# Kernel optimization log

Measured on AMD Instinct MI355X. Metric: run time of the kernel, lower is better.

## Reference

```python
import jax, jax.numpy as jnp
import numpy as np

B = 262144      # batch of states (PPO rollout)
J = 16          # num_pools -> state_dim=32, action_dim=256
M = 12          # num_epochs_per_day (experts)
H = 34          # hidden_dim (fixed in source)
A = J * J


def setup_inputs() -> dict:
    key = jax.random.key(0)
    ks = jax.random.split(key, 6)
    states = jax.random.normal(ks[0], (B, 2 * J), dtype=jnp.float32)
    epoch_idx = jax.random.randint(ks[1], (B,), 0, M, dtype=jnp.int32)
    # fc1: kaiming normal (relu), zero bias
    W1 = jax.random.normal(ks[2], (H, 2 * J), dtype=jnp.float32) * np.sqrt(2.0 / (2 * J))
    b1 = jnp.zeros((H,), dtype=jnp.float32)
    # m expert output layers [M, A, H]
    Wout = jax.random.normal(ks[3], (M, A, H), dtype=jnp.float32) * np.sqrt(1.0 / H)
    bout = jax.random.normal(ks[4], (M, A), dtype=jnp.float32) * np.sqrt(1.0 / H)
    mask = jax.random.randint(ks[5], (J, J), 0, 2, dtype=jnp.int32)
    return {"states": states, "epoch_idx": epoch_idx, "W1": W1, "b1": b1,
            "Wout": Wout, "bout": bout, "mask": mask}


def reference(states, epoch_idx, W1, b1, Wout, bout, mask):
    # shared trunk: [B, H]
    x = jax.nn.relu(jnp.einsum('bs,hs->bh', states, W1) + b1)
    # grouped expert GEMM via one-hot routing (equivalent to output_layers[epoch_idx])
    onehot = jax.nn.one_hot(epoch_idx, M, dtype=x.dtype)           # [B, M]
    xe = x[:, None, :] * onehot[:, :, None]                        # [B, M, H]
    logits = jnp.einsum('bmh,mah->ba', xe, Wout) + bout[epoch_idx]  # [B, A]
    logits = logits.reshape(-1, J, J)
    NEG = jnp.float32(-1e9)
    return jnp.where(mask == 0, NEG, logits)
```

## Files before the change

kernel.cpp:

```cpp
#include <hip/hip_runtime.h>

typedef __attribute__((ext_vector_type(8))) short short8;
typedef __attribute__((ext_vector_type(4))) float f32x4;
typedef __attribute__((ext_vector_type(4))) int   i32x4;

#define SDIM 32
#define HDIM 34
#define NEXP 12
#define ACOL 256
#define SPB  128
#define MAXROWS 320
#define STGS 260

#define BAR_LGKM() asm volatile("s_waitcnt lgkmcnt(0)\n\ts_barrier" ::: "memory")

__device__ __forceinline__ unsigned int bpack(float lo, float hi) {
    unsigned int a = __builtin_bit_cast(unsigned int, lo);
    unsigned int b = __builtin_bit_cast(unsigned int, hi);
    return ((a + 0x8000u) >> 16) | ((b + 0x8000u) & 0xffff0000u);
}

__global__ __launch_bounds__(256) void k0_wpack(
    const float* __restrict__ Wout, uint4* __restrict__ wpack,
    unsigned int* __restrict__ w2p)
{
    const int tid = blockIdx.x * 256 + threadIdx.x;
    if (tid >= NEXP * 4 * 4 * 64) return;
    const int lane = tid & 63;
    const int j    = (tid >> 6) & 3;
    const int wvv  = (tid >> 8) & 3;
    const int e    = tid >> 10;
    const int r = lane & 15, g = lane >> 4;
    const int col = wvv * 64 + j * 16 + r;
    const float* wr = Wout + ((size_t)e * ACOL + col) * HDIM;
    uint4 q;
    q.x = bpack(wr[g*8+0], wr[g*8+1]);
    q.y = bpack(wr[g*8+2], wr[g*8+3]);
    q.z = bpack(wr[g*8+4], wr[g*8+5]);
    q.w = bpack(wr[g*8+6], wr[g*8+7]);
    wpack[tid] = q;
    if (tid < NEXP * ACOL) {
        const float* wr2 = Wout + (size_t)tid * HDIM;
        w2p[tid] = bpack(wr2[32], wr2[33]);
    }
}

__global__ __launch_bounds__(256, 4) void actor_kernel(
    const float* __restrict__ states,
    const int*   __restrict__ epoch_idx,
    const float* __restrict__ W1,
    const float* __restrict__ b1,
    const uint4* __restrict__ wpack,
    const unsigned int* __restrict__ w2p,
    const float* __restrict__ bout,
    const int*   __restrict__ mask,
    float*       __restrict__ out,
    int nB)
{
    __shared__ __align__(16) unsigned int xs[MAXROWS * 16];
    __shared__ unsigned int   xt[MAXROWS];
    __shared__ unsigned short rowid[MAXROWS];
    __shared__ __align__(8) unsigned short stgb[16 * STGS];
    __shared__ int cnt[NEXP], goff[NEXP], ntl[NEXP];

    float* w1s = (float*)stgb;
    float* b1s = w1s + HDIM * SDIM;

    const int t  = threadIdx.x;
    const int s0 = blockIdx.x * SPB;

    for (int i = t; i < HDIM * SDIM; i += 256) w1s[i] = W1[i];
    if (t < HDIM) b1s[t] = b1[t];
    if (t < NEXP) cnt[t] = 0;
    for (int i = t; i < MAXROWS; i += 256) rowid[i] = 0xFFFFu;

    const int  sidx  = s0 + t;
    const bool valid = (t < SPB) && (sidx < nB);
    float sr[SDIM];
    int e = 0;
    if (valid) {
        const f32x4* sp = (const f32x4*)(states + (size_t)sidx * SDIM);
        #pragma unroll
        for (int q = 0; q < SDIM / 4; ++q) {
            f32x4 v = sp[q];
            sr[4*q+0] = v[0]; sr[4*q+1] = v[1]; sr[4*q+2] = v[2]; sr[4*q+3] = v[3];
        }
        e = epoch_idx[sidx];
    }
    __syncthreads();

    int rank = 0;
    if (valid) rank = atomicAdd(&cnt[e], 1);
    __syncthreads();

    if (t == 0) {
        int base = 0;
        #pragma unroll
        for (int i = 0; i < NEXP; ++i) {
            goff[i] = base;
            int nt = (cnt[i] + 15) >> 4;
            ntl[i] = nt;
            base += nt << 4;
        }
    }
    float x[HDIM];
    if (valid) {
        #pragma unroll 2
        for (int h = 0; h < HDIM; ++h) {
            float acc = b1s[h];
            const float4* wr = (const float4*)(w1s + h * SDIM);
            #pragma unroll
            for (int q = 0; q < SDIM / 4; ++q) {
                float4 wv = wr[q];
                acc = fmaf(sr[4*q+0], wv.x, acc);
                acc = fmaf(sr[4*q+1], wv.y, acc);
                acc = fmaf(sr[4*q+2], wv.z, acc);
                acc = fmaf(sr[4*q+3], wv.w, acc);
            }
            x[h] = fmaxf(acc, 0.0f);
        }
    }
    __syncthreads();

    if (valid) {
        const int slot = goff[e] + rank;
        const unsigned sw = (((unsigned)slot >> 2) & 3u) << 4;
        char* rbase = (char*)xs + slot * 64;
        unsigned d[17];
        #pragma unroll
        for (int k = 0; k < 17; ++k) d[k] = bpack(x[2*k], x[2*k+1]);
        #pragma unroll
        for (int c = 0; c < 4; ++c) {
            f32x4 q;
            q[0] = __builtin_bit_cast(float, d[4*c+0]);
            q[1] = __builtin_bit_cast(float, d[4*c+1]);
            q[2] = __builtin_bit_cast(float, d[4*c+2]);
            q[3] = __builtin_bit_cast(float, d[4*c+3]);
            *(f32x4*)(rbase + (((unsigned)(c * 16)) ^ sw)) = q;
        }
        xt[slot]    = bpack(x[32], x[33]);
        rowid[slot] = (unsigned short)t;
    }
    __syncthreads();

    const int wv   = t >> 6;
    const int lane = t & 63;
    const int r    = lane & 15;
    const int g    = lane >> 4;
    const int colbase = wv * 64 + r;
    const float NEG = -1e9f;
    const i32x4 mq = *(const i32x4*)(mask + 4 * lane);

    float* outb = out + (size_t)s0 * ACOL;

    for (int e2 = 0; e2 < NEXP; ++e2) {
        const int ntiles = ntl[e2];
        if (ntiles == 0) continue;

        short8   bf1[4];
        unsigned w2[4];
        const uint4* wp = wpack + ((size_t)(e2 * 4 + wv) * 4) * 64 + lane;
        #pragma unroll
        for (int j = 0; j < 4; ++j) {
            bf1[j] = __builtin_bit_cast(short8, wp[j * 64]);
            w2[j]  = (g == 0) ? w2p[e2 * ACOL + colbase + j * 16] : 0u;
        }
        const f32x4 bias4 = *(const f32x4*)(bout + e2 * ACOL + 4 * lane);

        const int tb = goff[e2];
        for (int st = 0; st < ntiles; ++st) {
            const int rb  = tb + (st << 4);
            const int row = rb + r;
            const unsigned sw = (((unsigned)row >> 2) & 3u) << 4;
            const char* rp = (const char*)xs + row * 64;
            short8 a1 = *(const short8*)(rp + (((unsigned)(g * 16)) ^ sw));
            short8 a2 = __builtin_bit_cast(short8,
                          make_uint4(g == 0 ? xt[row] : 0u, 0u, 0u, 0u));

            f32x4 acc[4];
            #pragma unroll
            for (int j = 0; j < 4; ++j) {
                f32x4 a = {0.f, 0.f, 0.f, 0.f};
                a = __builtin_amdgcn_mfma_f32_16x16x32_bf16(a1, bf1[j], a, 0, 0, 0);
                short8 b2 = __builtin_bit_cast(short8,
                              make_uint4(w2[j], 0u, 0u, 0u));
                a = __builtin_amdgcn_mfma_f32_16x16x32_bf16(a2, b2, a, 0, 0, 0);
                acc[j] = a;
            }

            BAR_LGKM();

            #pragma unroll
            for (int j = 0; j < 4; ++j) {
                const int c = colbase + 16 * j;
                #pragma unroll
                for (int i = 0; i < 4; ++i)
                    stgb[(g * 4 + i) * STGS + c] =
                        (unsigned short)bpack(acc[j][i], 0.0f);
            }

            BAR_LGKM();

            #pragma unroll
            for (int q = 0; q < 4; ++q) {
                const int lrow = wv * 4 + q;
                const unsigned rid = rowid[rb + lrow];
                const uint2 du = *(const uint2*)&stgb[lrow * STGS + 4 * lane];
                f32x4 v;
                v[0] = __builtin_bit_cast(float, du.x << 16)         + bias4[0];
                v[1] = __builtin_bit_cast(float, du.x & 0xffff0000u) + bias4[1];
                v[2] = __builtin_bit_cast(float, du.y << 16)         + bias4[2];
                v[3] = __builtin_bit_cast(float, du.y & 0xffff0000u) + bias4[3];
                v[0] = mq[0] ? v[0] : NEG;
                v[1] = mq[1] ? v[1] : NEG;
                v[2] = mq[2] ? v[2] : NEG;
                v[3] = mq[3] ? v[3] : NEG;
                if (rid != 0xFFFFu)
                    *(f32x4*)(outb + (size_t)rid * ACOL + 4 * lane) = v;
            }
        }
    }
}

extern "C" void kernel_launch(void* const* d_in, const int* in_sizes, int n_in,
                              void* d_out, int out_size, void* d_ws, size_t ws_size,
                              hipStream_t stream) {
    const float* states    = (const float*)d_in[0];
    const int*   epoch_idx = (const int*)  d_in[1];
    const float* W1        = (const float*)d_in[2];
    const float* b1        = (const float*)d_in[3];
    const float* Wout      = (const float*)d_in[4];
    const float* bout      = (const float*)d_in[5];
    const int*   mask      = (const int*)  d_in[6];
    float*       out       = (float*)d_out;

    const int nB   = in_sizes[0] / SDIM;
    const int grid = (nB + SPB - 1) / SPB;

    uint4*        wpack = (uint4*)d_ws;
    unsigned int* w2p   = (unsigned int*)((char*)d_ws + 196608);

    k0_wpack<<<48, 256, 0, stream>>>(Wout, wpack, w2p);
    actor_kernel<<<grid, 256, 0, stream>>>(states, epoch_idx, W1, b1,
                                           wpack, w2p, bout, mask, out, nB);
}
```

Baseline: 95.70 us.

## Process 256 states per block with 32-row expert tiles

Measured after the change: 98.87 us. +3.3%, slower.

```diff
diff --git a/kernel.cpp b/kernel.cpp
--- a/kernel.cpp
+++ b/kernel.cpp
@@ -8,8 +8,8 @@
 #define HDIM 34
 #define NEXP 12
 #define ACOL 256
-#define SPB  128
-#define MAXROWS 320
+#define SPB  256
+#define MAXROWS 640
 #define STGS 260
 
 #define BAR_LGKM() asm volatile("s_waitcnt lgkmcnt(0)\n\ts_barrier" ::: "memory")
@@ -45,7 +45,7 @@
     }
 }
 
-__global__ __launch_bounds__(256, 4) void actor_kernel(
+__global__ __launch_bounds__(256, 2) void actor_kernel(
     const float* __restrict__ states,
     const int*   __restrict__ epoch_idx,
     const float* __restrict__ W1,
@@ -60,7 +60,7 @@
     __shared__ __align__(16) unsigned int xs[MAXROWS * 16];
     __shared__ unsigned int   xt[MAXROWS];
     __shared__ unsigned short rowid[MAXROWS];
-    __shared__ __align__(8) unsigned short stgb[16 * STGS];
+    __shared__ __align__(8) unsigned short stgb[32 * STGS];
     __shared__ int cnt[NEXP], goff[NEXP], ntl[NEXP];
 
     float* w1s = (float*)stgb;
@@ -75,7 +75,7 @@
     for (int i = t; i < MAXROWS; i += 256) rowid[i] = 0xFFFFu;
 
     const int  sidx  = s0 + t;
-    const bool valid = (t < SPB) && (sidx < nB);
+    const bool valid = (sidx < nB);
     float sr[SDIM];
     int e = 0;
     if (valid) {
@@ -98,9 +98,9 @@
         #pragma unroll
         for (int i = 0; i < NEXP; ++i) {
             goff[i] = base;
-            int nt = (cnt[i] + 15) >> 4;
+            int nt = (cnt[i] + 31) >> 5;
             ntl[i] = nt;
-            base += nt << 4;
+            base += nt << 5;
         }
     }
     float x[HDIM];
@@ -169,23 +169,32 @@
 
         const int tb = goff[e2];
         for (int st = 0; st < ntiles; ++st) {
-            const int rb  = tb + (st << 4);
-            const int row = rb + r;
-            const unsigned sw = (((unsigned)row >> 2) & 3u) << 4;
-            const char* rp = (const char*)xs + row * 64;
-            short8 a1 = *(const short8*)(rp + (((unsigned)(g * 16)) ^ sw));
-            short8 a2 = __builtin_bit_cast(short8,
-                          make_uint4(g == 0 ? xt[row] : 0u, 0u, 0u, 0u));
-
-            f32x4 acc[4];
+            const int rb = tb + (st << 5);
+            const int rowA = rb + r, rowB = rb + 16 + r;
+            const unsigned swA = (((unsigned)rowA >> 2) & 3u) << 4;
+            const unsigned swB = (((unsigned)rowB >> 2) & 3u) << 4;
+            short8 a1A = *(const short8*)((const char*)xs + rowA * 64 +
+                                          (((unsigned)(g * 16)) ^ swA));
+            short8 a1B = *(const short8*)((const char*)xs + rowB * 64 +
+                                          (((unsigned)(g * 16)) ^ swB));
+            short8 a2A = __builtin_bit_cast(short8,
+                           make_uint4(g == 0 ? xt[rowA] : 0u, 0u, 0u, 0u));
+            short8 a2B = __builtin_bit_cast(short8,
+                           make_uint4(g == 0 ? xt[rowB] : 0u, 0u, 0u, 0u));
+
+            f32x4 accA[4], accB[4];
             #pragma unroll
             for (int j = 0; j < 4; ++j) {
-                f32x4 a = {0.f, 0.f, 0.f, 0.f};
-                a = __builtin_amdgcn_mfma_f32_16x16x32_bf16(a1, bf1[j], a, 0, 0, 0);
                 short8 b2 = __builtin_bit_cast(short8,
                               make_uint4(w2[j], 0u, 0u, 0u));
-                a = __builtin_amdgcn_mfma_f32_16x16x32_bf16(a2, b2, a, 0, 0, 0);
-                acc[j] = a;
+                f32x4 a = {0.f, 0.f, 0.f, 0.f};
+                a = __builtin_amdgcn_mfma_f32_16x16x32_bf16(a1A, bf1[j], a, 0, 0, 0);
+                a = __builtin_amdgcn_mfma_f32_16x16x32_bf16(a2A, b2, a, 0, 0, 0);
+                accA[j] = a;
+                f32x4 b = {0.f, 0.f, 0.f, 0.f};
+                b = __builtin_amdgcn_mfma_f32_16x16x32_bf16(a1B, bf1[j], b, 0, 0, 0);
+                b = __builtin_amdgcn_mfma_f32_16x16x32_bf16(a2B, b2, b, 0, 0, 0);
+                accB[j] = b;
             }
 
             BAR_LGKM();
@@ -194,16 +203,19 @@
             for (int j = 0; j < 4; ++j) {
                 const int c = colbase + 16 * j;
                 #pragma unroll
-                for (int i = 0; i < 4; ++i)
+                for (int i = 0; i < 4; ++i) {
                     stgb[(g * 4 + i) * STGS + c] =
-                        (unsigned short)bpack(acc[j][i], 0.0f);
+                        (unsigned short)bpack(accA[j][i], 0.0f);
+                    stgb[(16 + g * 4 + i) * STGS + c] =
+                        (unsigned short)bpack(accB[j][i], 0.0f);
+                }
             }
 
             BAR_LGKM();
 
             #pragma unroll
-            for (int q = 0; q < 4; ++q) {
-                const int lrow = wv * 4 + q;
+            for (int q = 0; q < 8; ++q) {
+                const int lrow = wv * 8 + q;
                 const unsigned rid = rowid[rb + lrow];
                 const uint2 du = *(const uint2*)&stgb[lrow * STGS + 4 * lane];
                 f32x4 v;
```
